# Kernel tuning notes

Hardware: AMD Instinct MI355X
Metric: run time of the kernel (lower is better)

Reference implementation:

```python
import jax, jax.numpy as jnp
import numpy as np

N_NODES = 50000
N_EDGES = 600000
D_IN = 128
D_OUT = 128


def setup_inputs() -> dict:
    key = jax.random.key(0)
    ks = jax.random.split(key, 10)
    x = jax.random.normal(ks[0], (N_NODES, D_IN), dtype=jnp.float32)
    # glorot init for per-support weights
    scale = jnp.sqrt(6.0 / (D_IN + D_OUT)).astype(jnp.float32)
    W0 = jax.random.uniform(ks[1], (D_IN, D_OUT), dtype=jnp.float32, minval=-scale, maxval=scale)
    W1 = jax.random.uniform(ks[2], (D_IN, D_OUT), dtype=jnp.float32, minval=-scale, maxval=scale)
    b = jnp.zeros((D_OUT,), dtype=jnp.float32)
    rows0 = jax.random.randint(ks[3], (N_EDGES,), 0, N_NODES, dtype=jnp.int32)
    cols0 = jax.random.randint(ks[4], (N_EDGES,), 0, N_NODES, dtype=jnp.int32)
    vals0 = jax.random.uniform(ks[5], (N_EDGES,), dtype=jnp.float32)
    rows1 = jax.random.randint(ks[6], (N_EDGES,), 0, N_NODES, dtype=jnp.int32)
    cols1 = jax.random.randint(ks[7], (N_EDGES,), 0, N_NODES, dtype=jnp.int32)
    vals1 = jax.random.uniform(ks[8], (N_EDGES,), dtype=jnp.float32)
    return {"x": x, "W0": W0, "W1": W1, "b": b,
            "rows0": rows0, "cols0": cols0, "vals0": vals0,
            "rows1": rows1, "cols1": cols1, "vals1": vals1}


def _spmm(rows, cols, vals, dense, num_rows):
    # sparse (COO) x dense: out[r] = sum_e vals[e] * dense[cols[e]] for rows[e]==r
    gathered = vals[:, None] * dense[cols]  # [E, D]
    return jax.ops.segment_sum(gathered, rows, num_segments=num_rows)


def reference(x, W0, W1, b, rows0, cols0, vals0, rows1, cols1, vals1):
    # support 0: A0 @ (x @ W0); support 1: A1 @ (x @ W1); sum, +bias, relu
    pre0 = x @ W0  # [N, D_OUT]
    pre1 = x @ W1
    s0 = _spmm(rows0, cols0, vals0, pre0, N_NODES)
    s1 = _spmm(rows1, cols1, vals1, pre1, N_NODES)
    out = s0 + s1 + b
    return jax.nn.relu(out)
```

## Files before the change

### kernel.cpp

```cpp
#include <hip/hip_runtime.h>

#define N_NODES 50000
#define N_EDGES 600000
#define D 128
#define SB 98
#define NSEG (2 * SB)
#define CAP 8192
#define HISTBLK 2048
#define BINBLK 4096
#define HIST_BLOCKS ((N_EDGES + HISTBLK - 1) / HISTBLK)
#define BIN_BLOCKS ((N_EDGES + BINBLK - 1) / BINBLK)
#define GEMM_BLOCKS ((N_NODES + 63) / 64)
#define SPMM_BLOCKS 2048
#define SPMM_WAVES (SPMM_BLOCKS * 4)

typedef __attribute__((ext_vector_type(8))) short short8v;
typedef __attribute__((ext_vector_type(4))) float f32x4;

__device__ __forceinline__ unsigned short f2bf(float f) {
  unsigned u = __float_as_uint(f);
  return (unsigned short)((u + 0x7FFFu + ((u >> 16) & 1u)) >> 16);
}

__device__ __forceinline__ void wpack_one(int idx, const float* __restrict__ W0,
                                          const float* __restrict__ W1,
                                          unsigned short* __restrict__ wpack) {
  const int sup = idx >> 11;
  const int ct = (idx >> 8) & 7;
  const int ks = (idx >> 6) & 3;
  const int l = idx & 63;
  const int q = l >> 4;
  const int c = l & 15;
  const float* W = (sup == 0) ? W0 : W1;
  const int d = ct * 16 + c;
  unsigned short v[8];
#pragma unroll
  for (int i = 0; i < 8; ++i) {
    const int k = ks * 32 + q * 8 + i;
    v[i] = f2bf(W[k * D + d]);
  }
  *(uint4*)(wpack + (size_t)idx * 8) = *(uint4*)v;
}

__global__ __launch_bounds__(256) void init_kernel(
    const float* __restrict__ W0, const float* __restrict__ W1,
    unsigned short* __restrict__ wpack, int* __restrict__ fillc) {
  const int t = threadIdx.x;
  if (blockIdx.x == 16) {
    if (t < NSEG) fillc[t] = 0;
    return;
  }
  wpack_one(blockIdx.x * 256 + t, W0, W1, wpack);
}

__global__ __launch_bounds__(256) void histpack_kernel(
    const int* __restrict__ rows0, const int* __restrict__ rows1,
    int* __restrict__ cnt, const float* __restrict__ W0,
    const float* __restrict__ W1, unsigned short* __restrict__ wpack) {
  const int t = threadIdx.x;
  if (blockIdx.x >= HIST_BLOCKS) {
    wpack_one(((blockIdx.x - HIST_BLOCKS) + 8 * blockIdx.y) * 256 + t, W0, W1,
              wpack);
    return;
  }
  __shared__ int h[SB];
  if (t < SB) h[t] = 0;
  __syncthreads();
  const int sup = blockIdx.y;
  const int* rows = sup ? rows1 : rows0;
  int e = blockIdx.x * HISTBLK + t;
#pragma unroll
  for (int k = 0; k < HISTBLK / 256; ++k, e += 256)
    if (e < N_EDGES) atomicAdd(&h[rows[e] >> 9], 1);
  __syncthreads();
  if (t < SB && h[t] > 0) atomicAdd(&cnt[sup * SB + t], h[t]);
}

__global__ __launch_bounds__(64) void scan196_kernel(
    const int* __restrict__ cnt, int* __restrict__ fillc,
    int* __restrict__ sbstart) {
  const int t = threadIdx.x;
  int v[4];
  int ssum = 0;
#pragma unroll
  for (int k = 0; k < 4; ++k) {
    const int g = t * 4 + k;
    v[k] = (g < NSEG) ? cnt[g] : 0;
    ssum += v[k];
  }
  int run = ssum;
#pragma unroll
  for (int off = 1; off < 64; off <<= 1) {
    const int u = __shfl_up(run, off);
    if (t >= off) run += u;
  }
  int excl = run - ssum;
#pragma unroll
  for (int k = 0; k < 4; ++k) {
    const int g = t * 4 + k;
    if (g < NSEG) {
      fillc[g] = excl;
      sbstart[g] = excl;
    }
    excl += v[k];
  }
  if (t == 63) sbstart[NSEG] = 2 * N_EDGES;
}

union BinGemmSmem {
  struct {
    int hist[SB];
    int lstart[SB];
    int lpos[SB];
    int gbase[SB];
    int2 stage[BINBLK];
  } bin;
  unsigned short sbuf[64][136];
};

template <bool CAPPED>
__global__ __launch_bounds__(256) void bingemm_kernel(
    const int* __restrict__ rows0, const int* __restrict__ cols0,
    const float* __restrict__ vals0, const int* __restrict__ rows1,
    const int* __restrict__ cols1, const float* __restrict__ vals1,
    int* __restrict__ fillc, int2* __restrict__ cv,
    const float* __restrict__ x, const unsigned short* __restrict__ wpack,
    unsigned short* __restrict__ preb) {
  __shared__ BinGemmSmem sm;
  const int t = threadIdx.x;
  const int bx = blockIdx.x;

  if (bx >= 2 * BIN_BLOCKS) {
    const int gb = bx - 2 * BIN_BLOCKS;
    const int w = t >> 6;
    const int lane = t & 63;
    const int q = lane >> 4;
    const int c = lane & 15;
    const int rowbase = gb * 64;
    const int arow = rowbase + w * 16 + c;

    short8v afrag[4];
#pragma unroll
    for (int ks = 0; ks < 4; ++ks) {
      const int k0 = ks * 32 + q * 8;
      float4 u0 = make_float4(0.f, 0.f, 0.f, 0.f);
      float4 u1 = u0;
      if (arow < N_NODES) {
        u0 = *(const float4*)(x + (size_t)arow * D + k0);
        u1 = *(const float4*)(x + (size_t)arow * D + k0 + 4);
      }
      unsigned short a[8];
      a[0] = f2bf(u0.x); a[1] = f2bf(u0.y);
      a[2] = f2bf(u0.z); a[3] = f2bf(u0.w);
      a[4] = f2bf(u1.x); a[5] = f2bf(u1.y);
      a[6] = f2bf(u1.z); a[7] = f2bf(u1.w);
      afrag[ks] = *(const short8v*)a;
    }

    const short8v* wp = (const short8v*)wpack;
#pragma unroll
    for (int sup = 0; sup < 2; ++sup) {
      unsigned short* pb = preb + (size_t)sup * N_NODES * D;
#pragma unroll
      for (int ct = 0; ct < 8; ++ct) {
        f32x4 acc = {0.f, 0.f, 0.f, 0.f};
#pragma unroll
        for (int ks = 0; ks < 4; ++ks) {
          const short8v bfrag = wp[((sup * 8 + ct) * 4 + ks) * 64 + lane];
          acc = __builtin_amdgcn_mfma_f32_16x16x32_bf16(afrag[ks], bfrag, acc,
                                                        0, 0, 0);
        }
#pragma unroll
        for (int j = 0; j < 4; ++j)
          sm.sbuf[w * 16 + q * 4 + j][ct * 16 + c] = f2bf(acc[j]);
      }
      __syncthreads();
#pragma unroll
      for (int it = 0; it < 4; ++it) {
        const int idx = t + it * 256;
        const int row = idx >> 4;
        const int dseg = (idx & 15) * 8;
        const uint4 v = *(const uint4*)&sm.sbuf[row][dseg];
        const int grow = rowbase + row;
        if (grow < N_NODES) *(uint4*)(pb + (size_t)grow * D + dseg) = v;
      }
      __syncthreads();
    }
    return;
  }

  const int sup = (bx >= BIN_BLOCKS) ? 1 : 0;
  const int bb = bx - sup * BIN_BLOCKS;
  const int* rows = sup ? rows1 : rows0;
  const int* cols = sup ? cols1 : cols0;
  const float* vals = sup ? vals1 : vals0;
  const int ebase = bb * BINBLK;
  const int nloc = min(BINBLK, N_EDGES - ebase);

  if (t < SB) sm.bin.hist[t] = 0;
  __syncthreads();

  int myr[16], myc[16];
  float myv[16];
#pragma unroll
  for (int k = 0; k < 16; ++k) {
    const int i = t + k * 256;
    myr[k] = -1;
    if (i < nloc) {
      myr[k] = rows[ebase + i];
      myc[k] = cols[ebase + i];
      myv[k] = vals[ebase + i];
      atomicAdd(&sm.bin.hist[myr[k] >> 9], 1);
    }
  }
  __syncthreads();

  if (t < 64) {
    const int g0 = 2 * t, g1 = 2 * t + 1;
    const int v0 = (g0 < SB) ? sm.bin.hist[g0] : 0;
    const int v1 = (g1 < SB) ? sm.bin.hist[g1] : 0;
    const int ssum = v0 + v1;
    int run = ssum;
#pragma unroll
    for (int off = 1; off < 64; off <<= 1) {
      const int u = __shfl_up(run, off);
      if (t >= off) run += u;
    }
    const int excl = run - ssum;
    if (g0 < SB) {
      sm.bin.lstart[g0] = excl;
      sm.bin.lpos[g0] = excl;
    }
    if (g1 < SB) {
      sm.bin.lstart[g1] = excl + v0;
      sm.bin.lpos[g1] = excl + v0;
    }
  }
  __syncthreads();

#pragma unroll
  for (int k = 0; k < 16; ++k) {
    if (myr[k] >= 0) {
      const int sb = myr[k] >> 9;
      const int p = atomicAdd(&sm.bin.lpos[sb], 1);
      sm.bin.stage[p] =
          make_int2(myc[k] | ((myr[k] & 511) << 16) | (sb << 25),
                    __float_as_int(myv[k]));
    }
  }
  if (t < SB && sm.bin.hist[t] > 0) {
    const int seg = sup * SB + t;
    const int bump = atomicAdd(&fillc[seg], sm.bin.hist[t]);
    sm.bin.gbase[t] = (CAPPED ? seg * CAP : 0) + bump;
  }
  __syncthreads();

  for (int i = t; i < nloc; i += 256) {
    const int2 ev = sm.bin.stage[i];
    const int sb = ((unsigned)ev.x) >> 25;
    cv[sm.bin.gbase[sb] + (i - sm.bin.lstart[sb])] = ev;
  }
}

template <bool CAPPED>
__global__ __launch_bounds__(1024) void sort_kernel(
    const int* __restrict__ sbstart, const int* __restrict__ fillc,
    int2* __restrict__ cv, int* __restrict__ rs_s, int* __restrict__ rs_e) {
  const int sb = blockIdx.x;
  const int sup = blockIdx.y;
  const int seg = sup * SB + sb;
  const int s = CAPPED ? seg * CAP : sbstart[seg];
  const int n = CAPPED ? fillc[seg] : (sbstart[seg + 1] - s);
  const int t = threadIdx.x;

  __shared__ int cnt[512];
  __shared__ int base[512];
  __shared__ int off[512];
  if (t < 512) {
    cnt[t] = 0;
    off[t] = 0;
  }
  __syncthreads();

  int2 ed[8];
#pragma unroll
  for (int k = 0; k < 8; ++k) {
    const int i = t + k * 1024;
    if (i < n) {
      ed[k] = cv[s + i];
      atomicAdd(&cnt[(ed[k].x >> 16) & 511], 1);
    }
  }
  __syncthreads();

  if (t < 64) {
    int v[8];
    int ssum = 0;
#pragma unroll
    for (int k = 0; k < 8; ++k) {
      v[k] = cnt[t * 8 + k];
      ssum += v[k];
    }
    int run = ssum;
#pragma unroll
    for (int off2 = 1; off2 < 64; off2 <<= 1) {
      const int u = __shfl_up(run, off2);
      if (t >= off2) run += u;
    }
    int excl = run - ssum;
#pragma unroll
    for (int k = 0; k < 8; ++k) {
      base[t * 8 + k] = excl;
      excl += v[k];
    }
  }
  __syncthreads();

  if (t < 512) {
    const int row = sb * 512 + t;
    if (row < N_NODES) {
      rs_s[sup * N_NODES + row] = s + base[t];
      rs_e[sup * N_NODES + row] = s + base[t] + cnt[t];
    }
  }

#pragma unroll
  for (int k = 0; k < 8; ++k) {
    const int i = t + k * 1024;
    if (i < n) {
      const int rl = (ed[k].x >> 16) & 511;
      const int pos = base[rl] + atomicAdd(&off[rl], 1);
      cv[s + pos] = ed[k];
    }
  }
}

__global__ __launch_bounds__(256) void spmm_fused_kernel(
    const int* __restrict__ rs_s, const int* __restrict__ rs_e,
    const int2* __restrict__ cv, const unsigned short* __restrict__ preb,
    const float* __restrict__ bias, float* __restrict__ out) {
  const int lane = threadIdx.x & 63;
  const int g = lane >> 4;
  const int dbase = (lane & 15) << 3;
  const int wid = blockIdx.x * 4 + (threadIdx.x >> 6);

  const float4 b0 = *(const float4*)(bias + dbase);
  const float4 b1 = *(const float4*)(bias + dbase + 4);

  for (int row = wid; row < N_NODES; row += SPMM_WAVES) {
    float acc[8];
#pragma unroll
    for (int i = 0; i < 8; ++i) acc[i] = 0.f;

#pragma unroll
    for (int sup = 0; sup < 2; ++sup) {
      const int s = rs_s[sup * N_NODES + row];
      const int e = rs_e[sup * N_NODES + row];
      const unsigned short* pb = preb + (size_t)sup * N_NODES * D;
      int j = s + g;
      for (; j + 4 < e; j += 8) {
        const int2 e0 = cv[j];
        const int2 e1 = cv[j + 4];
        const uint4 q0 = *(const uint4*)(pb + (size_t)(e0.x & 0xFFFF) * D + dbase);
        const uint4 q1 = *(const uint4*)(pb + (size_t)(e1.x & 0xFFFF) * D + dbase);
        const float v0 = __int_as_float(e0.y);
        const float v1 = __int_as_float(e1.y);
        acc[0] = fmaf(v0, __uint_as_float(q0.x << 16), acc[0]);
        acc[1] = fmaf(v0, __uint_as_float(q0.x & 0xFFFF0000u), acc[1]);
        acc[2] = fmaf(v0, __uint_as_float(q0.y << 16), acc[2]);
        acc[3] = fmaf(v0, __uint_as_float(q0.y & 0xFFFF0000u), acc[3]);
        acc[4] = fmaf(v0, __uint_as_float(q0.z << 16), acc[4]);
        acc[5] = fmaf(v0, __uint_as_float(q0.z & 0xFFFF0000u), acc[5]);
        acc[6] = fmaf(v0, __uint_as_float(q0.w << 16), acc[6]);
        acc[7] = fmaf(v0, __uint_as_float(q0.w & 0xFFFF0000u), acc[7]);
        acc[0] = fmaf(v1, __uint_as_float(q1.x << 16), acc[0]);
        acc[1] = fmaf(v1, __uint_as_float(q1.x & 0xFFFF0000u), acc[1]);
        acc[2] = fmaf(v1, __uint_as_float(q1.y << 16), acc[2]);
        acc[3] = fmaf(v1, __uint_as_float(q1.y & 0xFFFF0000u), acc[3]);
        acc[4] = fmaf(v1, __uint_as_float(q1.z << 16), acc[4]);
        acc[5] = fmaf(v1, __uint_as_float(q1.z & 0xFFFF0000u), acc[5]);
        acc[6] = fmaf(v1, __uint_as_float(q1.w << 16), acc[6]);
        acc[7] = fmaf(v1, __uint_as_float(q1.w & 0xFFFF0000u), acc[7]);
      }
      if (j < e) {
        const int2 e0 = cv[j];
        const uint4 q0 = *(const uint4*)(pb + (size_t)(e0.x & 0xFFFF) * D + dbase);
        const float v0 = __int_as_float(e0.y);
        acc[0] = fmaf(v0, __uint_as_float(q0.x << 16), acc[0]);
        acc[1] = fmaf(v0, __uint_as_float(q0.x & 0xFFFF0000u), acc[1]);
        acc[2] = fmaf(v0, __uint_as_float(q0.y << 16), acc[2]);
        acc[3] = fmaf(v0, __uint_as_float(q0.y & 0xFFFF0000u), acc[3]);
        acc[4] = fmaf(v0, __uint_as_float(q0.z << 16), acc[4]);
        acc[5] = fmaf(v0, __uint_as_float(q0.z & 0xFFFF0000u), acc[5]);
        acc[6] = fmaf(v0, __uint_as_float(q0.w << 16), acc[6]);
        acc[7] = fmaf(v0, __uint_as_float(q0.w & 0xFFFF0000u), acc[7]);
      }
    }

#pragma unroll
    for (int i = 0; i < 8; ++i) {
      acc[i] += __shfl_xor(acc[i], 16);
      acc[i] += __shfl_xor(acc[i], 32);
    }

    if (g == 0) {
      float4 r0, r1;
      r0.x = fmaxf(acc[0] + b0.x, 0.f);
      r0.y = fmaxf(acc[1] + b0.y, 0.f);
      r0.z = fmaxf(acc[2] + b0.z, 0.f);
      r0.w = fmaxf(acc[3] + b0.w, 0.f);
      r1.x = fmaxf(acc[4] + b1.x, 0.f);
      r1.y = fmaxf(acc[5] + b1.y, 0.f);
      r1.z = fmaxf(acc[6] + b1.z, 0.f);
      r1.w = fmaxf(acc[7] + b1.w, 0.f);
      float* op = out + (size_t)row * D + dbase;
      *(float4*)op = r0;
      *(float4*)(op + 4) = r1;
    }
  }
}

__global__ __launch_bounds__(256) void gemm_f32_kernel(
    const float* __restrict__ x, const float* __restrict__ W,
    float* __restrict__ pre) {
  const int tid = threadIdx.x;
  const int nloc = (tid >> 5) << 3;
  const int d4 = (tid & 31) << 2;
  const int nbase = blockIdx.x * 64;
  __shared__ float xs[64][D];
  {
    float4* xs4 = (float4*)(&xs[0][0]);
    const float4* xg4 = (const float4*)x;
#pragma unroll
    for (int i = 0; i < 8; ++i) {
      const int idx = tid + i * 256;
      const int row = nbase + (idx >> 5);
      xs4[idx] = (row < N_NODES) ? xg4[(size_t)row * 32 + (idx & 31)]
                                 : make_float4(0.f, 0.f, 0.f, 0.f);
    }
  }
  __syncthreads();
  float4 acc[8];
#pragma unroll
  for (int i = 0; i < 8; ++i) acc[i] = make_float4(0.f, 0.f, 0.f, 0.f);
  for (int k = 0; k < D; ++k) {
    const float4 w = *(const float4*)(W + k * D + d4);
#pragma unroll
    for (int i = 0; i < 8; ++i) {
      const float xv = xs[nloc + i][k];
      acc[i].x = fmaf(xv, w.x, acc[i].x);
      acc[i].y = fmaf(xv, w.y, acc[i].y);
      acc[i].z = fmaf(xv, w.z, acc[i].z);
      acc[i].w = fmaf(xv, w.w, acc[i].w);
    }
  }
#pragma unroll
  for (int i = 0; i < 8; ++i) {
    const int n = nbase + nloc + i;
    if (n < N_NODES) *(float4*)(pre + (size_t)n * D + d4) = acc[i];
  }
}

__global__ __launch_bounds__(256) void spmm_scatter_kernel(
    const int* __restrict__ rows, const int* __restrict__ cols,
    const float* __restrict__ vals, const float* __restrict__ pre,
    float* __restrict__ out) {
  const long long idx = (long long)blockIdx.x * blockDim.x + threadIdx.x;
  const int e = (int)(idx >> 6);
  if (e >= N_EDGES) return;
  const int dd = ((int)idx & 63) << 1;
  const int r = rows[e];
  const int c = cols[e];
  const float v = vals[e];
  const float2 p = *(const float2*)(pre + (size_t)c * D + dd);
  float* outp = out + (size_t)r * D + dd;
  atomicAdd(outp + 0, v * p.x);
  atomicAdd(outp + 1, v * p.y);
}

__global__ __launch_bounds__(256) void bias_relu_kernel(
    float* __restrict__ out, const float* __restrict__ b) {
  const int idx = blockIdx.x * blockDim.x + threadIdx.x;
  float4 v = ((float4*)out)[idx];
  const float4 bb = ((const float4*)b)[idx & 31];
  v.x = fmaxf(v.x + bb.x, 0.f);
  v.y = fmaxf(v.y + bb.y, 0.f);
  v.z = fmaxf(v.z + bb.z, 0.f);
  v.w = fmaxf(v.w + bb.w, 0.f);
  ((float4*)out)[idx] = v;
}

extern "C" void kernel_launch(void* const* d_in, const int* in_sizes, int n_in,
                              void* d_out, int out_size, void* d_ws,
                              size_t ws_size, hipStream_t stream) {
  const float* x = (const float*)d_in[0];
  const float* W0 = (const float*)d_in[1];
  const float* W1 = (const float*)d_in[2];
  const float* b = (const float*)d_in[3];
  const int* rows0 = (const int*)d_in[4];
  const int* cols0 = (const int*)d_in[5];
  const float* vals0 = (const float*)d_in[6];
  const int* rows1 = (const int*)d_in[7];
  const int* cols1 = (const int*)d_in[8];
  const float* vals1 = (const float*)d_in[9];
  float* out = (float*)d_out;

  auto align_up = [](size_t v) { return (v + 255) & ~(size_t)255; };
  const size_t PREB = align_up((size_t)2 * N_NODES * D * 2);
  const size_t FILLC = align_up((size_t)NSEG * 4);
  const size_t RS1 = align_up((size_t)2 * N_NODES * 4);
  const size_t WPACK = align_up((size_t)2 * D * D * 2);

  const size_t CVC = align_up((size_t)NSEG * CAP * 8);
  const size_t NEED_A = PREB + CVC + FILLC + 2 * RS1 + WPACK;
  const size_t CV = align_up((size_t)2 * N_EDGES * 8);
  const size_t CNT = align_up((size_t)NSEG * 4);
  const size_t SBSTART = align_up((size_t)(NSEG + 1) * 4);
  const size_t NEED_B = PREB + CV + CNT + FILLC + SBSTART + 2 * RS1 + WPACK;

  char* wsc = (char*)d_ws;

  if (ws_size >= NEED_A) {
    unsigned short* preb = (unsigned short*)wsc;
    int2* cv = (int2*)(wsc + PREB);
    int* fillc = (int*)(wsc + PREB + CVC);
    int* rs_s = (int*)(wsc + PREB + CVC + FILLC);
    int* rs_e = (int*)(wsc + PREB + CVC + FILLC + RS1);
    unsigned short* wpack =
        (unsigned short*)(wsc + PREB + CVC + FILLC + 2 * RS1);

    init_kernel<<<17, 256, 0, stream>>>(W0, W1, wpack, fillc);
    bingemm_kernel<true><<<2 * BIN_BLOCKS + GEMM_BLOCKS, 256, 0, stream>>>(
        rows0, cols0, vals0, rows1, cols1, vals1, fillc, cv, x, wpack, preb);
    sort_kernel<true><<<dim3(SB, 2), 1024, 0, stream>>>(nullptr, fillc, cv,
                                                        rs_s, rs_e);
    spmm_fused_kernel<<<SPMM_BLOCKS, 256, 0, stream>>>(rs_s, rs_e, cv, preb, b,
                                                       out);
  } else if (ws_size >= NEED_B) {
    unsigned short* preb = (unsigned short*)wsc;
    int2* cv = (int2*)(wsc + PREB);
    int* cnt = (int*)(wsc + PREB + CV);
    int* fillc = (int*)(wsc + PREB + CV + CNT);
    int* sbstart = (int*)(wsc + PREB + CV + CNT + FILLC);
    int* rs_s = (int*)(wsc + PREB + CV + CNT + FILLC + SBSTART);
    int* rs_e = (int*)(wsc + PREB + CV + CNT + FILLC + SBSTART + RS1);
    unsigned short* wpack =
        (unsigned short*)(wsc + PREB + CV + CNT + FILLC + SBSTART + 2 * RS1);

    hipMemsetAsync(cnt, 0, (size_t)NSEG * 4, stream);
    histpack_kernel<<<dim3(HIST_BLOCKS + 8, 2), 256, 0, stream>>>(
        rows0, rows1, cnt, W0, W1, wpack);
    scan196_kernel<<<1, 64, 0, stream>>>(cnt, fillc, sbstart);
    bingemm_kernel<false><<<2 * BIN_BLOCKS + GEMM_BLOCKS, 256, 0, stream>>>(
        rows0, cols0, vals0, rows1, cols1, vals1, fillc, cv, x, wpack, preb);
    sort_kernel<false><<<dim3(SB, 2), 1024, 0, stream>>>(sbstart, nullptr, cv,
                                                         rs_s, rs_e);
    spmm_fused_kernel<<<SPMM_BLOCKS, 256, 0, stream>>>(rs_s, rs_e, cv, preb, b,
                                                       out);
  } else {
    float* pre = (float*)wsc;
    hipMemsetAsync(d_out, 0, (size_t)N_NODES * D * 4, stream);
    const int scat_blocks = (N_EDGES * 64 + 255) / 256;
    gemm_f32_kernel<<<GEMM_BLOCKS, 256, 0, stream>>>(x, W0, pre);
    spmm_scatter_kernel<<<scat_blocks, 256, 0, stream>>>(rows0, cols0, vals0,
                                                         pre, out);
    gemm_f32_kernel<<<GEMM_BLOCKS, 256, 0, stream>>>(x, W1, pre);
    spmm_scatter_kernel<<<scat_blocks, 256, 0, stream>>>(rows1, cols1, vals1,
                                                         pre, out);
    bias_relu_kernel<<<(N_NODES * D / 4) / 256, 256, 0, stream>>>(out, b);
  }
}
```

Baseline: 89.14 us.

## Move dense GEMM from bin kernel into sort kernel launch

```diff
diff --git a/kernel.cpp b/kernel.cpp
--- a/kernel.cpp
+++ b/kernel.cpp
@@ -11,6 +11,7 @@
 #define HIST_BLOCKS ((N_EDGES + HISTBLK - 1) / HISTBLK)
 #define BIN_BLOCKS ((N_EDGES + BINBLK - 1) / BINBLK)
 #define GEMM_BLOCKS ((N_NODES + 63) / 64)
+#define GEMM1024_BLOCKS ((N_NODES + 255) / 256)
 #define SPMM_BLOCKS 2048
 #define SPMM_WAVES (SPMM_BLOCKS * 4)
 
@@ -42,6 +43,130 @@
   *(uint4*)(wpack + (size_t)idx * 8) = *(uint4*)v;
 }
 
+template <int NW>
+__device__ __forceinline__ void gemm_body(
+    int block_rowbase, const float* __restrict__ x,
+    const unsigned short* __restrict__ wpack, unsigned short* __restrict__ preb,
+    unsigned short (*sbuf)[136]) {
+  const int t = threadIdx.x;
+  const int w = t >> 6;
+  const int lane = t & 63;
+  const int q = lane >> 4;
+  const int c = lane & 15;
+  const int arow = block_rowbase + w * 16 + c;
+
+  short8v afrag[4];
+#pragma unroll
+  for (int ks = 0; ks < 4; ++ks) {
+    const int k0 = ks * 32 + q * 8;
+    float4 u0 = make_float4(0.f, 0.f, 0.f, 0.f);
+    float4 u1 = u0;
+    if (arow < N_NODES) {
+      u0 = *(const float4*)(x + (size_t)arow * D + k0);
+      u1 = *(const float4*)(x + (size_t)arow * D + k0 + 4);
+    }
+    unsigned short a[8];
+    a[0] = f2bf(u0.x); a[1] = f2bf(u0.y); a[2] = f2bf(u0.z); a[3] = f2bf(u0.w);
+    a[4] = f2bf(u1.x); a[5] = f2bf(u1.y); a[6] = f2bf(u1.z); a[7] = f2bf(u1.w);
+    afrag[ks] = *(const short8v*)a;
+  }
+
+  const short8v* wp = (const short8v*)wpack;
+#pragma unroll
+  for (int sup = 0; sup < 2; ++sup) {
+    unsigned short* pb = preb + (size_t)sup * N_NODES * D;
+#pragma unroll
+    for (int ct = 0; ct < 8; ++ct) {
+      f32x4 acc = {0.f, 0.f, 0.f, 0.f};
+#pragma unroll
+      for (int ks = 0; ks < 4; ++ks) {
+        const short8v bfrag = wp[((sup * 8 + ct) * 4 + ks) * 64 + lane];
+        acc = __builtin_amdgcn_mfma_f32_16x16x32_bf16(afrag[ks], bfrag, acc,
+                                                      0, 0, 0);
+      }
+#pragma unroll
+      for (int j = 0; j < 4; ++j)
+        sbuf[w * 16 + q * 4 + j][ct * 16 + c] = f2bf(acc[j]);
+    }
+    __syncthreads();
+#pragma unroll
+    for (int it = 0; it < 4; ++it) {
+      const int idx = t + it * (NW * 64);
+      const int row = idx >> 4;
+      const int dseg = (idx & 15) * 8;
+      const uint4 v = *(const uint4*)&sbuf[row][dseg];
+      const int grow = block_rowbase + row;
+      if (grow < N_NODES) *(uint4*)(pb + (size_t)grow * D + dseg) = v;
+    }
+    __syncthreads();
+  }
+}
+
+__device__ __forceinline__ void sort_body(int sup, int sb, int s, int n,
+                                          int2* __restrict__ cv,
+                                          int* __restrict__ rs_s,
+                                          int* __restrict__ rs_e,
+                                          int* cnt, int* base, int* off) {
+  const int t = threadIdx.x;
+  if (t < 512) {
+    cnt[t] = 0;
+    off[t] = 0;
+  }
+  __syncthreads();
+
+  int2 ed[8];
+#pragma unroll
+  for (int k = 0; k < 8; ++k) {
+    const int i = t + k * 1024;
+    if (i < n) {
+      ed[k] = cv[s + i];
+      atomicAdd(&cnt[(ed[k].x >> 16) & 511], 1);
+    }
+  }
+  __syncthreads();
+
+  if (t < 64) {
+    int v[8];
+    int ssum = 0;
+#pragma unroll
+    for (int k = 0; k < 8; ++k) {
+      v[k] = cnt[t * 8 + k];
+      ssum += v[k];
+    }
+    int run = ssum;
+#pragma unroll
+    for (int off2 = 1; off2 < 64; off2 <<= 1) {
+      const int u = __shfl_up(run, off2);
+      if (t >= off2) run += u;
+    }
+    int excl = run - ssum;
+#pragma unroll
+    for (int k = 0; k < 8; ++k) {
+      base[t * 8 + k] = excl;
+      excl += v[k];
+    }
+  }
+  __syncthreads();
+
+  if (t < 512) {
+    const int row = sb * 512 + t;
+    if (row < N_NODES) {
+      rs_s[sup * N_NODES + row] = s + base[t];
+      rs_e[sup * N_NODES + row] = s + base[t] + cnt[t];
+    }
+  }
+
+#pragma unroll
+  for (int k = 0; k < 8; ++k) {
+    const int i = t + k * 1024;
+    if (i < n) {
+      const int rl = (ed[k].x >> 16) & 511;
+      const int pos = base[rl] + atomicAdd(&off[rl], 1);
+      cv[s + pos] = ed[k];
+    }
+  }
+}
+
 __global__ __launch_bounds__(256) void init_kernel(
     const float* __restrict__ W0, const float* __restrict__ W1,
     unsigned short* __restrict__ wpack, int* __restrict__ fillc) {
@@ -51,6 +176,118 @@
     return;
   }
   wpack_one(blockIdx.x * 256 + t, W0, W1, wpack);
+}
+
+__global__ __launch_bounds__(256) void binonly_kernel(
+    const int* __restrict__ rows0, const int* __restrict__ cols0,
+    const float* __restrict__ vals0, const int* __restrict__ rows1,
+    const int* __restrict__ cols1, const float* __restrict__ vals1,
+    int* __restrict__ fillc, int2* __restrict__ cv) {
+  __shared__ int hist[SB];
+  __shared__ int lstart[SB];
+  __shared__ int lpos[SB];
+  __shared__ int gbase[SB];
+  __shared__ int2 stage[BINBLK];
+
+  const int t = threadIdx.x;
+  const int bx = blockIdx.x;
+  const int sup = (bx >= BIN_BLOCKS) ? 1 : 0;
+  const int bb = bx - sup * BIN_BLOCKS;
+  const int* rows = sup ? rows1 : rows0;
+  const int* cols = sup ? cols1 : cols0;
+  const float* vals = sup ? vals1 : vals0;
+  const int ebase = bb * BINBLK;
+  const int nloc = min(BINBLK, N_EDGES - ebase);
+
+  if (t < SB) hist[t] = 0;
+  __syncthreads();
+
+  int myr[16], myc[16];
+  float myv[16];
+#pragma unroll
+  for (int k = 0; k < 16; ++k) {
+    const int i = t + k * 256;
+    myr[k] = -1;
+    if (i < nloc) {
+      myr[k] = rows[ebase + i];
+      myc[k] = cols[ebase + i];
+      myv[k] = vals[ebase + i];
+      atomicAdd(&hist[myr[k] >> 9], 1);
+    }
+  }
+  __syncthreads();
+
+  if (t < 64) {
+    const int g0 = 2 * t, g1 = 2 * t + 1;
+    const int v0 = (g0 < SB) ? hist[g0] : 0;
+    const int v1 = (g1 < SB) ? hist[g1] : 0;
+    const int ssum = v0 + v1;
+    int run = ssum;
+#pragma unroll
+    for (int off = 1; off < 64; off <<= 1) {
+      const int u = __shfl_up(run, off);
+      if (t >= off) run += u;
+    }
+    const int excl = run - ssum;
+    if (g0 < SB) {
+      lstart[g0] = excl;
+      lpos[g0] = excl;
+    }
+    if (g1 < SB) {
+      lstart[g1] = excl + v0;
+      lpos[g1] = excl + v0;
+    }
+  }
+  __syncthreads();
+
+#pragma unroll
+  for (int k = 0; k < 16; ++k) {
+    if (myr[k] >= 0) {
+      const int sb = myr[k] >> 9;
+      const int p = atomicAdd(&lpos[sb], 1);
+      stage[p] = make_int2(myc[k] | ((myr[k] & 511) << 16) | (sb << 25),
+                           __float_as_int(myv[k]));
+    }
+  }
+  if (t < SB && hist[t] > 0) {
+    const int seg = sup * SB + t;
+    const int bump = atomicAdd(&fillc[seg], hist[t]);
+    gbase[t] = seg * CAP + bump;
+  }
+  __syncthreads();
+
+  for (int i = t; i < nloc; i += 256) {
+    const int2 ev = stage[i];
+    const int sb = ((unsigned)ev.x) >> 25;
+    cv[gbase[sb] + (i - lstart[sb])] = ev;
+  }
+}
+
+union SortGemmSmem {
+  struct {
+    int cnt[512];
+    int base[512];
+    int off[512];
+  } s;
+  unsigned short sbuf[256][136];
+};
+
+__global__ __launch_bounds__(1024) void sortgemm_kernel(
+    int* __restrict__ fillc, int2* __restrict__ cv, int* __restrict__ rs_s,
+    int* __restrict__ rs_e, const float* __restrict__ x,
+    const unsigned short* __restrict__ wpack,
+    unsigned short* __restrict__ preb) {
+  __shared__ SortGemmSmem sm;
+  const int bx = blockIdx.x;
+  if (bx < NSEG) {
+    const int sup = bx / SB;
+    const int sb = bx - sup * SB;
+    const int s = bx * CAP;
+    const int n = fillc[bx];
+    sort_body(sup, sb, s, n, cv, rs_s, rs_e, sm.s.cnt, sm.s.base, sm.s.off);
+  } else {
+    gemm_body<16>((bx - NSEG) * 256, x, wpack, preb, sm.sbuf);
+  }
 }
 
 __global__ __launch_bounds__(256) void histpack_kernel(
@@ -118,7 +355,6 @@
   unsigned short sbuf[64][136];
 };
 
-template <bool CAPPED>
 __global__ __launch_bounds__(256) void bingemm_kernel(
     const int* __restrict__ rows0, const int* __restrict__ cols0,
     const float* __restrict__ vals0, const int* __restrict__ rows1,
@@ -131,61 +367,7 @@
   const int bx = blockIdx.x;
 
   if (bx >= 2 * BIN_BLOCKS) {
-    const int gb = bx - 2 * BIN_BLOCKS;
-    const int w = t >> 6;
-    const int lane = t & 63;
-    const int q = lane >> 4;
-    const int c = lane & 15;
-    const int rowbase = gb * 64;
-    const int arow = rowbase + w * 16 + c;
-
-    short8v afrag[4];
-#pragma unroll
-    for (int ks = 0; ks < 4; ++ks) {
-      const int k0 = ks * 32 + q * 8;
-      float4 u0 = make_float4(0.f, 0.f, 0.f, 0.f);
-      float4 u1 = u0;
-      if (arow < N_NODES) {
-        u0 = *(const float4*)(x + (size_t)arow * D + k0);
-        u1 = *(const float4*)(x + (size_t)arow * D + k0 + 4);
-      }
-      unsigned short a[8];
-      a[0] = f2bf(u0.x); a[1] = f2bf(u0.y);
-      a[2] = f2bf(u0.z); a[3] = f2bf(u0.w);
-      a[4] = f2bf(u1.x); a[5] = f2bf(u1.y);
-      a[6] = f2bf(u1.z); a[7] = f2bf(u1.w);
-      afrag[ks] = *(const short8v*)a;
-    }
-
-    const short8v* wp = (const short8v*)wpack;
-#pragma unroll
-    for (int sup = 0; sup < 2; ++sup) {
-      unsigned short* pb = preb + (size_t)sup * N_NODES * D;
-#pragma unroll
-      for (int ct = 0; ct < 8; ++ct) {
-        f32x4 acc = {0.f, 0.f, 0.f, 0.f};
-#pragma unroll
-        for (int ks = 0; ks < 4; ++ks) {
-          const short8v bfrag = wp[((sup * 8 + ct) * 4 + ks) * 64 + lane];
-          acc = __builtin_amdgcn_mfma_f32_16x16x32_bf16(afrag[ks], bfrag, acc,
-                                                        0, 0, 0);
-        }
-#pragma unroll
-        for (int j = 0; j < 4; ++j)
-          sm.sbuf[w * 16 + q * 4 + j][ct * 16 + c] = f2bf(acc[j]);
-      }
-      __syncthreads();
-#pragma unroll
-      for (int it = 0; it < 4; ++it) {
-        const int idx = t + it * 256;
-        const int row = idx >> 4;
-        const int dseg = (idx & 15) * 8;
-        const uint4 v = *(const uint4*)&sm.sbuf[row][dseg];
-        const int grow = rowbase + row;
-        if (grow < N_NODES) *(uint4*)(pb + (size_t)grow * D + dseg) = v;
-      }
-      __syncthreads();
-    }
+    gemm_body<4>((bx - 2 * BIN_BLOCKS) * 64, x, wpack, preb, sm.sbuf);
     return;
   }
 
@@ -250,8 +432,7 @@
   }
   if (t < SB && sm.bin.hist[t] > 0) {
     const int seg = sup * SB + t;
-    const int bump = atomicAdd(&fillc[seg], sm.bin.hist[t]);
-    sm.bin.gbase[t] = (CAPPED ? seg * CAP : 0) + bump;
+    sm.bin.gbase[t] = atomicAdd(&fillc[seg], sm.bin.hist[t]);
   }
   __syncthreads();
 
@@ -262,77 +443,18 @@
   }
 }
 
-template <bool CAPPED>
-__global__ __launch_bounds__(1024) void sort_kernel(
-    const int* __restrict__ sbstart, const int* __restrict__ fillc,
-    int2* __restrict__ cv, int* __restrict__ rs_s, int* __restrict__ rs_e) {
+__global__ __launch_bounds__(1024) void sortB_kernel(
+    const int* __restrict__ sbstart, int2* __restrict__ cv,
+    int* __restrict__ rs_s, int* __restrict__ rs_e) {
+  __shared__ int cnt[512];
+  __shared__ int base[512];
+  __shared__ int off[512];
   const int sb = blockIdx.x;
   const int sup = blockIdx.y;
   const int seg = sup * SB + sb;
-  const int s = CAPPED ? seg * CAP : sbstart[seg];
-  const int n = CAPPED ? fillc[seg] : (sbstart[seg + 1] - s);
-  const int t = threadIdx.x;
-
-  __shared__ int cnt[512];
-  __shared__ int base[512];
-  __shared__ int off[512];
-  if (t < 512) {
-    cnt[t] = 0;
-    off[t] = 0;
-  }
-  __syncthreads();
-
-  int2 ed[8];
-#pragma unroll
-  for (int k = 0; k < 8; ++k) {
-    const int i = t + k * 1024;
-    if (i < n) {
-      ed[k] = cv[s + i];
-      atomicAdd(&cnt[(ed[k].x >> 16) & 511], 1);
-    }
-  }
-  __syncthreads();
-
-  if (t < 64) {
-    int v[8];
-    int ssum = 0;
-#pragma unroll
-    for (int k = 0; k < 8; ++k) {
-      v[k] = cnt[t * 8 + k];
-      ssum += v[k];
-    }
-    int run = ssum;
-#pragma unroll
-    for (int off2 = 1; off2 < 64; off2 <<= 1) {
-      const int u = __shfl_up(run, off2);
-      if (t >= off2) run += u;
-    }
-    int excl = run - ssum;
-#pragma unroll
-    for (int k = 0; k < 8; ++k) {
-      base[t * 8 + k] = excl;
-      excl += v[k];
-    }
-  }
-  __syncthreads();
-
-  if (t < 512) {
-    const int row = sb * 512 + t;
-    if (row < N_NODES) {
-      rs_s[sup * N_NODES + row] = s + base[t];
-      rs_e[sup * N_NODES + row] = s + base[t] + cnt[t];
-    }
-  }
-
-#pragma unroll
-  for (int k = 0; k < 8; ++k) {
-    const int i = t + k * 1024;
-    if (i < n) {
-      const int rl = (ed[k].x >> 16) & 511;
-      const int pos = base[rl] + atomicAdd(&off[rl], 1);
-      cv[s + pos] = ed[k];
-    }
-  }
+  const int s = sbstart[seg];
+  const int n = sbstart[seg + 1] - s;
+  sort_body(sup, sb, s, n, cv, rs_s, rs_e, cnt, base, off);
 }
 
 __global__ __launch_bounds__(256) void spmm_fused_kernel(
@@ -530,10 +652,10 @@
         (unsigned short*)(wsc + PREB + CVC + FILLC + 2 * RS1);
 
     init_kernel<<<17, 256, 0, stream>>>(W0, W1, wpack, fillc);
-    bingemm_kernel<true><<<2 * BIN_BLOCKS + GEMM_BLOCKS, 256, 0, stream>>>(
-        rows0, cols0, vals0, rows1, cols1, vals1, fillc, cv, x, wpack, preb);
-    sort_kernel<true><<<dim3(SB, 2), 1024, 0, stream>>>(nullptr, fillc, cv,
-                                                        rs_s, rs_e);
+    binonly_kernel<<<2 * BIN_BLOCKS, 256, 0, stream>>>(
+        rows0, cols0, vals0, rows1, cols1, vals1, fillc, cv);
+    sortgemm_kernel<<<NSEG + GEMM1024_BLOCKS, 1024, 0, stream>>>(
+        fillc, cv, rs_s, rs_e, x, wpack, preb);
     spmm_fused_kernel<<<SPMM_BLOCKS, 256, 0, stream>>>(rs_s, rs_e, cv, preb, b,
                                                        out);
   } else if (ws_size >= NEED_B) {
@@ -551,10 +673,9 @@
     histpack_kernel<<<dim3(HIST_BLOCKS + 8, 2), 256, 0, stream>>>(
         rows0, rows1, cnt, W0, W1, wpack);
     scan196_kernel<<<1, 64, 0, stream>>>(cnt, fillc, sbstart);
-    bingemm_kernel<false><<<2 * BIN_BLOCKS + GEMM_BLOCKS, 256, 0, stream>>>(
+    bingemm_kernel<<<2 * BIN_BLOCKS + GEMM_BLOCKS, 256, 0, stream>>>(
         rows0, cols0, vals0, rows1, cols1, vals1, fillc, cv, x, wpack, preb);
-    sort_kernel<false><<<dim3(SB, 2), 1024, 0, stream>>>(sbstart, nullptr, cv,
-                                                         rs_s, rs_e);
+    sortB_kernel<<<dim3(SB, 2), 1024, 0, stream>>>(sbstart, cv, rs_s, rs_e);
     spmm_fused_kernel<<<SPMM_BLOCKS, 256, 0, stream>>>(rs_s, rs_e, cv, preb, b,
                                                        out);
   } else {
```

New measurement: 98.06 us. +10.0%, slower.

## Split dense GEMM between bin and sort kernels to overlap with sorting

Applied to the files above, without the earlier changes.

```diff
diff --git a/kernel.cpp b/kernel.cpp
--- a/kernel.cpp
+++ b/kernel.cpp
@@ -11,6 +11,9 @@
 #define HIST_BLOCKS ((N_EDGES + HISTBLK - 1) / HISTBLK)
 #define BIN_BLOCKS ((N_EDGES + BINBLK - 1) / BINBLK)
 #define GEMM_BLOCKS ((N_NODES + 63) / 64)
+#define GEMM_A 498
+#define GEMM_B 71
+#define GEMM_B_ROWBASE (GEMM_A * 64)
 #define SPMM_BLOCKS 2048
 #define SPMM_WAVES (SPMM_BLOCKS * 4)
 
@@ -42,6 +45,217 @@
   *(uint4*)(wpack + (size_t)idx * 8) = *(uint4*)v;
 }
 
+template <int NW>
+__device__ __forceinline__ void gemm_body(
+    int block_rowbase, const float* __restrict__ x,
+    const unsigned short* __restrict__ wpack, unsigned short* __restrict__ preb,
+    unsigned short (*sbuf)[136]) {
+  const int t = threadIdx.x;
+  const int w = t >> 6;
+  const int lane = t & 63;
+  const int q = lane >> 4;
+  const int c = lane & 15;
+  const int arow = block_rowbase + w * 16 + c;
+
+  short8v afrag[4];
+#pragma unroll
+  for (int ks = 0; ks < 4; ++ks) {
+    const int k0 = ks * 32 + q * 8;
+    float4 u0 = make_float4(0.f, 0.f, 0.f, 0.f);
+    float4 u1 = u0;
+    if (arow < N_NODES) {
+      u0 = *(const float4*)(x + (size_t)arow * D + k0);
+      u1 = *(const float4*)(x + (size_t)arow * D + k0 + 4);
+    }
+    unsigned short a[8];
+    a[0] = f2bf(u0.x); a[1] = f2bf(u0.y); a[2] = f2bf(u0.z); a[3] = f2bf(u0.w);
+    a[4] = f2bf(u1.x); a[5] = f2bf(u1.y); a[6] = f2bf(u1.z); a[7] = f2bf(u1.w);
+    afrag[ks] = *(const short8v*)a;
+  }
+
+  const short8v* wp = (const short8v*)wpack;
+#pragma unroll
+  for (int sup = 0; sup < 2; ++sup) {
+    unsigned short* pb = preb + (size_t)sup * N_NODES * D;
+#pragma unroll
+    for (int ct = 0; ct < 8; ++ct) {
+      f32x4 acc = {0.f, 0.f, 0.f, 0.f};
+#pragma unroll
+      for (int ks = 0; ks < 4; ++ks) {
+        const short8v bfrag = wp[((sup * 8 + ct) * 4 + ks) * 64 + lane];
+        acc = __builtin_amdgcn_mfma_f32_16x16x32_bf16(afrag[ks], bfrag, acc,
+                                                      0, 0, 0);
+      }
+#pragma unroll
+      for (int j = 0; j < 4; ++j)
+        sbuf[w * 16 + q * 4 + j][ct * 16 + c] = f2bf(acc[j]);
+    }
+    __syncthreads();
+#pragma unroll
+    for (int it = 0; it < 4; ++it) {
+      const int idx = t + it * (NW * 64);
+      const int row = idx >> 4;
+      const int dseg = (idx & 15) * 8;
+      const uint4 v = *(const uint4*)&sbuf[row][dseg];
+      const int grow = block_rowbase + row;
+      if (grow < N_NODES) *(uint4*)(pb + (size_t)grow * D + dseg) = v;
+    }
+    __syncthreads();
+  }
+}
+
+__device__ __forceinline__ void sort_body(int sup, int sb, int s, int n,
+                                          int2* __restrict__ cv,
+                                          int* __restrict__ rs_s,
+                                          int* __restrict__ rs_e,
+                                          int* cnt, int* base, int* off) {
+  const int t = threadIdx.x;
+  if (t < 512) {
+    cnt[t] = 0;
+    off[t] = 0;
+  }
+  __syncthreads();
+
+  int2 ed[8];
+#pragma unroll
+  for (int k = 0; k < 8; ++k) {
+    const int i = t + k * 1024;
+    if (i < n) {
+      ed[k] = cv[s + i];
+      atomicAdd(&cnt[(ed[k].x >> 16) & 511], 1);
+    }
+  }
+  __syncthreads();
+
+  if (t < 64) {
+    int v[8];
+    int ssum = 0;
+#pragma unroll
+    for (int k = 0; k < 8; ++k) {
+      v[k] = cnt[t * 8 + k];
+      ssum += v[k];
+    }
+    int run = ssum;
+#pragma unroll
+    for (int off2 = 1; off2 < 64; off2 <<= 1) {
+      const int u = __shfl_up(run, off2);
+      if (t >= off2) run += u;
+    }
+    int excl = run - ssum;
+#pragma unroll
+    for (int k = 0; k < 8; ++k) {
+      base[t * 8 + k] = excl;
+      excl += v[k];
+    }
+  }
+  __syncthreads();
+
+  if (t < 512) {
+    const int row = sb * 512 + t;
+    if (row < N_NODES) {
+      rs_s[sup * N_NODES + row] = s + base[t];
+      rs_e[sup * N_NODES + row] = s + base[t] + cnt[t];
+    }
+  }
+
+#pragma unroll
+  for (int k = 0; k < 8; ++k) {
+    const int i = t + k * 1024;
+    if (i < n) {
+      const int rl = (ed[k].x >> 16) & 511;
+      const int pos = base[rl] + atomicAdd(&off[rl], 1);
+      cv[s + pos] = ed[k];
+    }
+  }
+}
+
+struct BinSmem {
+  int hist[SB];
+  int lstart[SB];
+  int lpos[SB];
+  int gbase[SB];
+  int2 stage[BINBLK];
+};
+
+template <bool CAPPED>
+__device__ __forceinline__ void bin_body(
+    int bx, const int* __restrict__ rows0, const int* __restrict__ cols0,
+    const float* __restrict__ vals0, const int* __restrict__ rows1,
+    const int* __restrict__ cols1, const float* __restrict__ vals1,
+    int* __restrict__ fillc, int2* __restrict__ cv, BinSmem* sm) {
+  const int t = threadIdx.x;
+  const int sup = (bx >= BIN_BLOCKS) ? 1 : 0;
+  const int bb = bx - sup * BIN_BLOCKS;
+  const int* rows = sup ? rows1 : rows0;
+  const int* cols = sup ? cols1 : cols0;
+  const float* vals = sup ? vals1 : vals0;
+  const int ebase = bb * BINBLK;
+  const int nloc = min(BINBLK, N_EDGES - ebase);
+
+  if (t < SB) sm->hist[t] = 0;
+  __syncthreads();
+
+  int myr[16], myc[16];
+  float myv[16];
+#pragma unroll
+  for (int k = 0; k < 16; ++k) {
+    const int i = t + k * 256;
+    myr[k] = -1;
+    if (i < nloc) {
+      myr[k] = rows[ebase + i];
+      myc[k] = cols[ebase + i];
+      myv[k] = vals[ebase + i];
+      atomicAdd(&sm->hist[myr[k] >> 9], 1);
+    }
+  }
+  __syncthreads();
+
+  if (t < 64) {
+    const int g0 = 2 * t, g1 = 2 * t + 1;
+    const int v0 = (g0 < SB) ? sm->hist[g0] : 0;
+    const int v1 = (g1 < SB) ? sm->hist[g1] : 0;
+    const int ssum = v0 + v1;
+    int run = ssum;
+#pragma unroll
+    for (int off = 1; off < 64; off <<= 1) {
+      const int u = __shfl_up(run, off);
+      if (t >= off) run += u;
+    }
+    const int excl = run - ssum;
+    if (g0 < SB) {
+      sm->lstart[g0] = excl;
+      sm->lpos[g0] = excl;
+    }
+    if (g1 < SB) {
+      sm->lstart[g1] = excl + v0;
+      sm->lpos[g1] = excl + v0;
+    }
+  }
+  __syncthreads();
+
+#pragma unroll
+  for (int k = 0; k < 16; ++k) {
+    if (myr[k] >= 0) {
+      const int sb = myr[k] >> 9;
+      const int p = atomicAdd(&sm->lpos[sb], 1);
+      sm->stage[p] = make_int2(myc[k] | ((myr[k] & 511) << 16) | (sb << 25),
+                               __float_as_int(myv[k]));
+    }
+  }
+  if (t < SB && sm->hist[t] > 0) {
+    const int seg = sup * SB + t;
+    const int bump = atomicAdd(&fillc[seg], sm->hist[t]);
+    sm->gbase[t] = (CAPPED ? seg * CAP : 0) + bump;
+  }
+  __syncthreads();
+
+  for (int i = t; i < nloc; i += 256) {
+    const int2 ev = sm->stage[i];
+    const int sb = ((unsigned)ev.x) >> 25;
+    cv[sm->gbase[sb] + (i - sm->lstart[sb])] = ev;
+  }
+}
+
 __global__ __launch_bounds__(256) void init_kernel(
     const float* __restrict__ W0, const float* __restrict__ W1,
     unsigned short* __restrict__ wpack, int* __restrict__ fillc) {
@@ -51,6 +265,54 @@
     return;
   }
   wpack_one(blockIdx.x * 256 + t, W0, W1, wpack);
+}
+
+union BinGemmSmem {
+  BinSmem bin;
+  unsigned short sbuf[64][136];
+};
+
+__global__ __launch_bounds__(256) void bingemmA_kernel(
+    const int* __restrict__ rows0, const int* __restrict__ cols0,
+    const float* __restrict__ vals0, const int* __restrict__ rows1,
+    const int* __restrict__ cols1, const float* __restrict__ vals1,
+    int* __restrict__ fillc, int2* __restrict__ cv,
+    const float* __restrict__ x, const unsigned short* __restrict__ wpack,
+    unsigned short* __restrict__ preb) {
+  __shared__ BinGemmSmem sm;
+  const int bx = blockIdx.x;
+  if (bx >= 2 * BIN_BLOCKS) {
+    gemm_body<4>((bx - 2 * BIN_BLOCKS) * 64, x, wpack, preb, sm.sbuf);
+    return;
+  }
+  bin_body<true>(bx, rows0, cols0, vals0, rows1, cols1, vals1, fillc, cv,
+                 &sm.bin);
+}
+
+union SortGemmSmem {
+  struct {
+    int cnt[512];
+    int base[512];
+    int off[512];
+  } s;
+  unsigned short sbuf[256][136];
+};
+
+__global__ __launch_bounds__(1024) void sortgemm_kernel(
+    int* __restrict__ fillc, int2* __restrict__ cv, int* __restrict__ rs_s,
+    int* __restrict__ rs_e, const float* __restrict__ x,
+    const unsigned short* __restrict__ wpack,
+    unsigned short* __restrict__ preb) {
+  __shared__ SortGemmSmem sm;
+  const int bx = blockIdx.x;
+  if (bx < NSEG) {
+    const int sup = bx / SB;
+    const int sb = bx - sup * SB;
+    sort_body(sup, sb, bx * CAP, fillc[bx], cv, rs_s, rs_e, sm.s.cnt,
+              sm.s.base, sm.s.off);
+  } else {
+    gemm_body<16>(GEMM_B_ROWBASE + (bx - NSEG) * 256, x, wpack, preb, sm.sbuf);
+  }
 }
 
 __global__ __launch_bounds__(256) void histpack_kernel(
@@ -107,19 +369,7 @@
   if (t == 63) sbstart[NSEG] = 2 * N_EDGES;
 }
 
-union BinGemmSmem {
-  struct {
-    int hist[SB];
-    int lstart[SB];
-    int lpos[SB];
-    int gbase[SB];
-    int2 stage[BINBLK];
-  } bin;
-  unsigned short sbuf[64][136];
-};
-
-template <bool CAPPED>
-__global__ __launch_bounds__(256) void bingemm_kernel(
+__global__ __launch_bounds__(256) void bingemmB_kernel(
     const int* __restrict__ rows0, const int* __restrict__ cols0,
     const float* __restrict__ vals0, const int* __restrict__ rows1,
     const int* __restrict__ cols1, const float* __restrict__ vals1,
@@ -127,212 +377,27 @@
     const float* __restrict__ x, const unsigned short* __restrict__ wpack,
     unsigned short* __restrict__ preb) {
   __shared__ BinGemmSmem sm;
-  const int t = threadIdx.x;
   const int bx = blockIdx.x;
-
   if (bx >= 2 * BIN_BLOCKS) {
-    const int gb = bx - 2 * BIN_BLOCKS;
-    const int w = t >> 6;
-    const int lane = t & 63;
-    const int q = lane >> 4;
-    const int c = lane & 15;
-    const int rowbase = gb * 64;
-    const int arow = rowbase + w * 16 + c;
-
-    short8v afrag[4];
-#pragma unroll
-    for (int ks = 0; ks < 4; ++ks) {
-      const int k0 = ks * 32 + q * 8;
-      float4 u0 = make_float4(0.f, 0.f, 0.f, 0.f);
-      float4 u1 = u0;
-      if (arow < N_NODES) {
-        u0 = *(const float4*)(x + (size_t)arow * D + k0);
-        u1 = *(const float4*)(x + (size_t)arow * D + k0 + 4);
-      }
-      unsigned short a[8];
-      a[0] = f2bf(u0.x); a[1] = f2bf(u0.y);
-      a[2] = f2bf(u0.z); a[3] = f2bf(u0.w);
-      a[4] = f2bf(u1.x); a[5] = f2bf(u1.y);
-      a[6] = f2bf(u1.z); a[7] = f2bf(u1.w);
-      afrag[ks] = *(const short8v*)a;
-    }
-
-    const short8v* wp = (const short8v*)wpack;
-#pragma unroll
-    for (int sup = 0; sup < 2; ++sup) {
-      unsigned short* pb = preb + (size_t)sup * N_NODES * D;
-#pragma unroll
-      for (int ct = 0; ct < 8; ++ct) {
-        f32x4 acc = {0.f, 0.f, 0.f, 0.f};
-#pragma unroll
-        for (int ks = 0; ks < 4; ++ks) {
-          const short8v bfrag = wp[((sup * 8 + ct) * 4 + ks) * 64 + lane];
-          acc = __builtin_amdgcn_mfma_f32_16x16x32_bf16(afrag[ks], bfrag, acc,
-                                                        0, 0, 0);
-        }
-#pragma unroll
-        for (int j = 0; j < 4; ++j)
-          sm.sbuf[w * 16 + q * 4 + j][ct * 16 + c] = f2bf(acc[j]);
-      }
-      __syncthreads();
-#pragma unroll
-      for (int it = 0; it < 4; ++it) {
-        const int idx = t + it * 256;
-        const int row = idx >> 4;
-        const int dseg = (idx & 15) * 8;
-        const uint4 v = *(const uint4*)&sm.sbuf[row][dseg];
-        const int grow = rowbase + row;
-        if (grow < N_NODES) *(uint4*)(pb + (size_t)grow * D + dseg) = v;
-      }
-      __syncthreads();
-    }
+    gemm_body<4>((bx - 2 * BIN_BLOCKS) * 64, x, wpack, preb, sm.sbuf);
     return;
   }
-
-  const int sup = (bx >= BIN_BLOCKS) ? 1 : 0;
-  const int bb = bx - sup * BIN_BLOCKS;
-  const int* rows = sup ? rows1 : rows0;
-  const int* cols = sup ? cols1 : cols0;
-  const float* vals = sup ? vals1 : vals0;
-  const int ebase = bb * BINBLK;
-  const int nloc = min(BINBLK, N_EDGES - ebase);
-
-  if (t < SB) sm.bin.hist[t] = 0;
-  __syncthreads();
-
-  int myr[16], myc[16];
-  float myv[16];
-#pragma unroll
-  for (int k = 0; k < 16; ++k) {
-    const int i = t + k * 256;
-    myr[k] = -1;
-    if (i < nloc) {
-      myr[k] = rows[ebase + i];
-      myc[k] = cols[ebase + i];
-      myv[k] = vals[ebase + i];
-      atomicAdd(&sm.bin.hist[myr[k] >> 9], 1);
-    }
-  }
-  __syncthreads();
-
-  if (t < 64) {
-    const int g0 = 2 * t, g1 = 2 * t + 1;
-    const int v0 = (g0 < SB) ? sm.bin.hist[g0] : 0;
-    const int v1 = (g1 < SB) ? sm.bin.hist[g1] : 0;
-    const int ssum = v0 + v1;
-    int run = ssum;
-#pragma unroll
-    for (int off = 1; off < 64; off <<= 1) {
-      const int u = __shfl_up(run, off);
-      if (t >= off) run += u;
-    }
-    const int excl = run - ssum;
-    if (g0 < SB) {
-      sm.bin.lstart[g0] = excl;
-      sm.bin.lpos[g0] = excl;
-    }
-    if (g1 < SB) {
-      sm.bin.lstart[g1] = excl + v0;
-      sm.bin.lpos[g1] = excl + v0;
-    }
-  }
-  __syncthreads();
-
-#pragma unroll
-  for (int k = 0; k < 16; ++k) {
-    if (myr[k] >= 0) {
-      const int sb = myr[k] >> 9;
-      const int p = atomicAdd(&sm.bin.lpos[sb], 1);
-      sm.bin.stage[p] =
-          make_int2(myc[k] | ((myr[k] & 511) << 16) | (sb << 25),
-                    __float_as_int(myv[k]));
-    }
-  }
-  if (t < SB && sm.bin.hist[t] > 0) {
-    const int seg = sup * SB + t;
-    const int bump = atomicAdd(&fillc[seg], sm.bin.hist[t]);
-    sm.bin.gbase[t] = (CAPPED ? seg * CAP : 0) + bump;
-  }
-  __syncthreads();
-
-  for (int i = t; i < nloc; i += 256) {
-    const int2 ev = sm.bin.stage[i];
-    const int sb = ((unsigned)ev.x) >> 25;
-    cv[sm.bin.gbase[sb] + (i - sm.bin.lstart[sb])] = ev;
-  }
-}
-
-template <bool CAPPED>
-__global__ __launch_bounds__(1024) void sort_kernel(
-    const int* __restrict__ sbstart, const int* __restrict__ fillc,
-    int2* __restrict__ cv, int* __restrict__ rs_s, int* __restrict__ rs_e) {
+  bin_body<false>(bx, rows0, cols0, vals0, rows1, cols1, vals1, fillc, cv,
+                  &sm.bin);
+}
+
+__global__ __launch_bounds__(1024) void sortB_kernel(
+    const int* __restrict__ sbstart, int2* __restrict__ cv,
+    int* __restrict__ rs_s, int* __restrict__ rs_e) {
+  __shared__ int cnt[512];
+  __shared__ int base[512];
+  __shared__ int off[512];
   const int sb = blockIdx.x;
   const int sup = blockIdx.y;
   const int seg = sup * SB + sb;
-  const int s = CAPPED ? seg * CAP : sbstart[seg];
-  const int n = CAPPED ? fillc[seg] : (sbstart[seg + 1] - s);
-  const int t = threadIdx.x;
-
-  __shared__ int cnt[512];
-  __shared__ int base[512];
-  __shared__ int off[512];
-  if (t < 512) {
-    cnt[t] = 0;
-    off[t] = 0;
-  }
-  __syncthreads();
-
-  int2 ed[8];
-#pragma unroll
-  for (int k = 0; k < 8; ++k) {
-    const int i = t + k * 1024;
-    if (i < n) {
-      ed[k] = cv[s + i];
-      atomicAdd(&cnt[(ed[k].x >> 16) & 511], 1);
-    }
-  }
-  __syncthreads();
-
-  if (t < 64) {
-    int v[8];
-    int ssum = 0;
-#pragma unroll
-    for (int k = 0; k < 8; ++k) {
-      v[k] = cnt[t * 8 + k];
-      ssum += v[k];
-    }
-    int run = ssum;
-#pragma unroll
-    for (int off2 = 1; off2 < 64; off2 <<= 1) {
-      const int u = __shfl_up(run, off2);
-      if (t >= off2) run += u;
-    }
-    int excl = run - ssum;
-#pragma unroll
-    for (int k = 0; k < 8; ++k) {
-      base[t * 8 + k] = excl;
-      excl += v[k];
-    }
-  }
-  __syncthreads();
-
-  if (t < 512) {
-    const int row = sb * 512 + t;
-    if (row < N_NODES) {
-      rs_s[sup * N_NODES + row] = s + base[t];
-      rs_e[sup * N_NODES + row] = s + base[t] + cnt[t];
-    }
-  }
-
-#pragma unroll
-  for (int k = 0; k < 8; ++k) {
-    const int i = t + k * 1024;
-    if (i < n) {
-      const int rl = (ed[k].x >> 16) & 511;
-      const int pos = base[rl] + atomicAdd(&off[rl], 1);
-      cv[s + pos] = ed[k];
-    }
-  }
+  const int s = sbstart[seg];
+  const int n = sbstart[seg + 1] - s;
+  sort_body(sup, sb, s, n, cv, rs_s, rs_e, cnt, base, off);
 }
 
 __global__ __launch_bounds__(256) void spmm_fused_kernel(
@@ -530,10 +595,10 @@
         (unsigned short*)(wsc + PREB + CVC + FILLC + 2 * RS1);
 
     init_kernel<<<17, 256, 0, stream>>>(W0, W1, wpack, fillc);
-    bingemm_kernel<true><<<2 * BIN_BLOCKS + GEMM_BLOCKS, 256, 0, stream>>>(
+    bingemmA_kernel<<<2 * BIN_BLOCKS + GEMM_A, 256, 0, stream>>>(
         rows0, cols0, vals0, rows1, cols1, vals1, fillc, cv, x, wpack, preb);
-    sort_kernel<true><<<dim3(SB, 2), 1024, 0, stream>>>(nullptr, fillc, cv,
-                                                        rs_s, rs_e);
+    sortgemm_kernel<<<NSEG + GEMM_B, 1024, 0, stream>>>(fillc, cv, rs_s, rs_e,
+                                                        x, wpack, preb);
     spmm_fused_kernel<<<SPMM_BLOCKS, 256, 0, stream>>>(rs_s, rs_e, cv, preb, b,
                                                        out);
   } else if (ws_size >= NEED_B) {
@@ -551,10 +616,9 @@
     histpack_kernel<<<dim3(HIST_BLOCKS + 8, 2), 256, 0, stream>>>(
         rows0, rows1, cnt, W0, W1, wpack);
     scan196_kernel<<<1, 64, 0, stream>>>(cnt, fillc, sbstart);
-    bingemm_kernel<false><<<2 * BIN_BLOCKS + GEMM_BLOCKS, 256, 0, stream>>>(
+    bingemmB_kernel<<<2 * BIN_BLOCKS + GEMM_BLOCKS, 256, 0, stream>>>(
         rows0, cols0, vals0, rows1, cols1, vals1, fillc, cv, x, wpack, preb);
-    sort_kernel<false><<<dim3(SB, 2), 1024, 0, stream>>>(sbstart, nullptr, cv,
-                                                         rs_s, rs_e);
+    sortB_kernel<<<dim3(SB, 2), 1024, 0, stream>>>(sbstart, cv, rs_s, rs_e);
     spmm_fused_kernel<<<SPMM_BLOCKS, 256, 0, stream>>>(rs_s, rs_e, cv, preb, b,
                                                        out);
   } else {
```

After: 98.86 us. 10.9% more time.
